# Kernel optimization log

Measured on AMD Instinct MI355X. Metric: run time of the kernel, lower is better.

## Reference

```python
import jax, jax.numpy as jnp
import numpy as np

TOPK = 0.1  # fraction of h*w spatial positions, from __init__ default


def setup_inputs() -> dict:
    key = jax.random.key(0)
    x = jax.random.normal(key, (32, 256, 56, 56), dtype=jnp.float32)
    return {"x": x}


def reference(x) -> jnp.ndarray:
    # Faithful translation of TopKLayer.sparse_hw (including its quirky
    # comparison of ascending *ranks* against the spatial *index* of the
    # k-th largest element, exactly as the torch code does).
    n, c, h, w = x.shape
    k = int(max(1, TOPK * h * w))  # topk_keep_num = 313 for 56x56
    x_r = x.reshape(n * c, h * w)              # (nc, hw)
    abs_x = jnp.abs(x_r)
    # ranks[i, j] = ascending rank of abs_x[i, j] within row i
    ranks = jnp.argsort(jnp.argsort(abs_x, axis=1), axis=1)
    # spatial index of the k-th largest |x| in each row
    thr_idx = jax.lax.top_k(abs_x, k)[1][:, -1]  # (nc,)
    mask = (ranks < thr_idx[:, None]).reshape(n, c, h, w)
    return x * mask.astype(x.dtype)
```

## Files before the change

### kernel.cpp

```cpp
#include <hip/hip_runtime.h>
#include <stdint.h>


#define HW   3136
#define NT   256
#define KSEL 313u
#define NB0  2048
#define SP0  (NB0 / NT)
#define CAP  512

__device__ __forceinline__ unsigned block_scan_incl(unsigned v, unsigned* wt) {
    const int lane = threadIdx.x & 63;
    const int w = threadIdx.x >> 6;
    for (int d = 1; d < 64; d <<= 1) {
        unsigned o = __shfl_up(v, d, 64);
        if (lane >= d) v += o;
    }
    if (lane == 63) wt[w] = v;
    __syncthreads();
    unsigned add = 0;
    for (int i = 0; i < w; ++i) add += wt[i];
    __syncthreads();
    return v + add;
}

template <bool fromTop>
__device__ void locate0(const unsigned* hist, unsigned rank,
                        unsigned* wt, unsigned* s_b) {
    const int t = threadIdx.x;
    const int base = t * SP0;
    unsigned g = 0;
#pragma unroll
    for (int i = 0; i < SP0; ++i) {
        int b = fromTop ? (NB0 - 1 - (base + i)) : (base + i);
        g += hist[b];
    }
    unsigned S = block_scan_incl(g, wt);
    if (S >= rank && (S - g) < rank) {
        unsigned lr = rank - (S - g);
        unsigned acc = 0;
        for (int i = 0; i < SP0; ++i) {
            int b = fromTop ? (NB0 - 1 - (base + i)) : (base + i);
            unsigned h = hist[b];
            acc += h;
            if (acc >= lr) { s_b[0] = (unsigned)b; s_b[1] = lr - (acc - h); break; }
        }
    }
    if (t == 0) s_b[3] = 0;
    __syncthreads();
}

template <bool fromTop>
__device__ void select_stable(const uint4* s_x4, const unsigned* hist0,
                              unsigned* cand, unsigned* wt, unsigned* s_b,
                              unsigned rank, unsigned& keyOut, unsigned& eOut) {
    const int t = threadIdx.x;
    locate0<fromTop>(hist0, rank, wt, s_b);
    const unsigned b0 = s_b[0];
    const unsigned m  = s_b[1];

    for (int j = t; j < HW / 4; j += NT) {
        uint4 v = s_x4[j];
        const unsigned i0 = 4u * (unsigned)j;
        unsigned k;
        k = v.x & 0x7fffffffu;
        if ((k >> 20) == b0) { unsigned p = atomicAdd(&s_b[3], 1u); if (p < CAP) cand[p] = ((k & 0xFFFFFu) << 12) | i0; }
        k = v.y & 0x7fffffffu;
        if ((k >> 20) == b0) { unsigned p = atomicAdd(&s_b[3], 1u); if (p < CAP) cand[p] = ((k & 0xFFFFFu) << 12) | (i0 + 1u); }
        k = v.z & 0x7fffffffu;
        if ((k >> 20) == b0) { unsigned p = atomicAdd(&s_b[3], 1u); if (p < CAP) cand[p] = ((k & 0xFFFFFu) << 12) | (i0 + 2u); }
        k = v.w & 0x7fffffffu;
        if ((k >> 20) == b0) { unsigned p = atomicAdd(&s_b[3], 1u); if (p < CAP) cand[p] = ((k & 0xFFFFFu) << 12) | (i0 + 3u); }
    }
    __syncthreads();
    const unsigned cnt = s_b[3];

    if (cnt <= CAP) {
        for (int i = t; i < (int)cnt; i += NT) {
            const unsigned ci = cand[i];
            const unsigned Ci = fromTop ? (ci ^ 0xFFFu) : ci;
            unsigned r = 1;
            for (int j = 0; j < (int)cnt; ++j) {
                const unsigned Cj = fromTop ? (cand[j] ^ 0xFFFu) : cand[j];
                if (fromTop ? (Cj > Ci) : (Cj < Ci)) r++;
            }
            if (r == m) s_b[2] = ci;
        }
        __syncthreads();
        const unsigned ci = s_b[2];
        keyOut = (b0 << 20) | (ci >> 12);
        eOut = ci & 0xFFFu;
    } else {
        const unsigned* s_x = (const unsigned*)s_x4;
        for (int j = t; j < HW; j += NT) {
            const unsigned k = s_x[j] & 0x7fffffffu;
            if ((k >> 20) != b0) continue;
            unsigned Ci = ((k & 0xFFFFFu) << 12) | (unsigned)j;
            if (fromTop) Ci ^= 0xFFFu;
            unsigned r = 1;
            for (int j2 = 0; j2 < HW; ++j2) {
                const unsigned k2 = s_x[j2] & 0x7fffffffu;
                if ((k2 >> 20) != b0) continue;
                unsigned Cj = ((k2 & 0xFFFFFu) << 12) | (unsigned)j2;
                if (fromTop) Cj ^= 0xFFFu;
                if (fromTop ? (Cj > Ci) : (Cj < Ci)) r++;
            }
            if (r == m) s_b[2] = ((k & 0xFFFFFu) << 12) | (unsigned)j;
        }
        __syncthreads();
        const unsigned ci = s_b[2];
        keyOut = (b0 << 20) | (ci >> 12);
        eOut = ci & 0xFFFu;
    }
}

extern "C" __global__ void __launch_bounds__(NT)
topk_kernel(const float* __restrict__ x, float* __restrict__ out) {
    __shared__ uint4 s_x4[HW / 4];
    __shared__ unsigned s_hist0[NB0];
    __shared__ unsigned s_cand[CAP];
    __shared__ unsigned s_wt[4];
    __shared__ unsigned s_b[4];

    const int t = threadIdx.x;
    const int row = blockIdx.x;
    const uint4* __restrict__ xin = (const uint4*)(x + (size_t)row * HW);
    uint4* __restrict__ xout = (uint4*)(out + (size_t)row * HW);

    for (int i = t; i < NB0; i += NT) s_hist0[i] = 0;
    __syncthreads();
    for (int j = t; j < HW / 4; j += NT) {
        uint4 v = xin[j];
        s_x4[j] = v;
        atomicAdd(&s_hist0[(v.x & 0x7fffffffu) >> 20], 1u);
        atomicAdd(&s_hist0[(v.y & 0x7fffffffu) >> 20], 1u);
        atomicAdd(&s_hist0[(v.z & 0x7fffffffu) >> 20], 1u);
        atomicAdd(&s_hist0[(v.w & 0x7fffffffu) >> 20], 1u);
    }
    __syncthreads();

    unsigned KA, tIdx;
    select_stable<true>(s_x4, s_hist0, s_cand, s_wt, s_b, KSEL, KA, tIdx);

    if (tIdx == 0) {
        uint4 z = make_uint4(0u, 0u, 0u, 0u);
        for (int j = t; j < HW / 4; j += NT) xout[j] = z;
        return;
    }

    unsigned KB, eB;
    select_stable<false>(s_x4, s_hist0, s_cand, s_wt, s_b, tIdx, KB, eB);

    for (int j = t; j < HW / 4; j += NT) {
        uint4 v = s_x4[j];
        const unsigned i0 = 4u * (unsigned)j;
        unsigned k;
        k = v.x & 0x7fffffffu; if (!(k < KB || (k == KB && i0      <= eB))) v.x = 0u;
        k = v.y & 0x7fffffffu; if (!(k < KB || (k == KB && i0 + 1u <= eB))) v.y = 0u;
        k = v.z & 0x7fffffffu; if (!(k < KB || (k == KB && i0 + 2u <= eB))) v.z = 0u;
        k = v.w & 0x7fffffffu; if (!(k < KB || (k == KB && i0 + 3u <= eB))) v.w = 0u;
        xout[j] = v;
    }
}

extern "C" void kernel_launch(void* const* d_in, const int* in_sizes, int n_in,
                              void* d_out, int out_size, void* d_ws, size_t ws_size,
                              hipStream_t stream) {
    const float* x = (const float*)d_in[0];
    float* out = (float*)d_out;
    const int rows = in_sizes[0] / HW;
    topk_kernel<<<dim3(rows), dim3(NT), 0, stream>>>(x, out);
}
```

Before: 71.59 us.

## Process one row per wavefront with packed 16-bit histograms and global re-reads

Each row's selection now runs on a single 64-lane wavefront, with four rows per block, instead of a 256-thread block per row. The row is no longer staged in LDS; global memory is re-read on each pass. Histogram counters are packed as 16-bit pairs with padding, and the selection uses wave-level scans and ballots instead of block barriers, plus a second-level histogram to narrow the candidates. The goal is to remove __syncthreads and cut LDS per row so more rows are in flight. In exchange the input is read from global several times per row.

Result: slower. 97.40 us (+36.1%).

```diff
diff --git a/kernel.cpp b/kernel.cpp
--- a/kernel.cpp
+++ b/kernel.cpp
@@ -2,164 +2,258 @@
 #include <stdint.h>
 
 
-#define HW   3136
-#define NT   256
-#define KSEL 313u
-#define NB0  2048
-#define SP0  (NB0 / NT)
-#define CAP  512
-
-__device__ __forceinline__ unsigned block_scan_incl(unsigned v, unsigned* wt) {
-    const int lane = threadIdx.x & 63;
-    const int w = threadIdx.x >> 6;
+#define HW     3136
+#define NW4    784
+#define WPB    4
+#define NT     256
+#define KSEL   313u
+#define NB0WP  1088
+#define NB2WP  136
+#define CAP    320
+#define CAP2   64
+
+#define OFF_H0   0
+#define OFF_CAND 1088
+#define OFF_H2   1408
+#define OFF_CNT  1544
+#define OFF_SCR  1545
+#define OFF_TINY 1546
+#define WW       1616
+
+#define PADW(w) ((w) + ((w) >> 4))
+
+__device__ __forceinline__ unsigned wscan(unsigned v) {
+    const int lane = threadIdx.x & 63;
+#pragma unroll
     for (int d = 1; d < 64; d <<= 1) {
         unsigned o = __shfl_up(v, d, 64);
         if (lane >= d) v += o;
     }
-    if (lane == 63) wt[w] = v;
-    __syncthreads();
-    unsigned add = 0;
-    for (int i = 0; i < w; ++i) add += wt[i];
-    __syncthreads();
-    return v + add;
+    return v;
+}
+
+__device__ __forceinline__ unsigned h16(const unsigned* h, unsigned bin) {
+    unsigned w = h[PADW(bin >> 1)];
+    return (bin & 1) ? (w >> 16) : (w & 0xFFFFu);
+}
+
+__device__ __forceinline__ void hadd(unsigned* h, unsigned bin) {
+    atomicAdd((unsigned*)&h[PADW(bin >> 1)], (bin & 1) ? 0x10000u : 1u);
+}
+
+template <int SEGW, bool fromTop>
+__device__ void locate(const unsigned* h, unsigned m, unsigned& bOut, unsigned& mOut) {
+    const int lane = threadIdx.x & 63;
+    const int seg = fromTop ? (63 - lane) : lane;
+    unsigned s = 0;
+#pragma unroll
+    for (int i = 0; i < SEGW; ++i) {
+        unsigned w = h[PADW(seg * SEGW + i)];
+        s += (w & 0xFFFFu) + (w >> 16);
+    }
+    unsigned S = wscan(s);
+    unsigned long long bal = __ballot(S >= m);
+    int fl = __ffsll(bal) - 1;
+    unsigned packed = 0;
+    if (lane == fl) {
+        unsigned rem = m - (S - s);
+        unsigned acc = 0;
+        const int nb = SEGW * 2;
+        for (int i = 0; i < nb; ++i) {
+            unsigned bin = fromTop ? (unsigned)(seg * nb + nb - 1 - i)
+                                   : (unsigned)(seg * nb + i);
+            unsigned hh = h16(h, bin);
+            acc += hh;
+            if (acc >= rem) { packed = (bin << 16) | (rem - (acc - hh)); break; }
+        }
+    }
+    packed = __shfl(packed, fl, 64);
+    bOut = packed >> 16;
+    mOut = packed & 0xFFFFu;
+}
+
+__device__ unsigned occ_scan(unsigned* wl, const uint4* xin, unsigned K, unsigned mm) {
+    const int lane = threadIdx.x & 63;
+    unsigned prev = 0;
+    for (int it = 0; it < 13; ++it) {
+        int j = it * 64 + lane;
+        unsigned lm = 0;
+        if (j < NW4) {
+            uint4 v = xin[j];
+            lm  = ((v.x & 0x7fffffffu) == K) ? 1u : 0u;
+            lm |= ((v.y & 0x7fffffffu) == K) ? 2u : 0u;
+            lm |= ((v.z & 0x7fffffffu) == K) ? 4u : 0u;
+            lm |= ((v.w & 0x7fffffffu) == K) ? 8u : 0u;
+        }
+        unsigned c = __popc(lm);
+        unsigned S = wscan(c);
+        unsigned tot = __shfl(S, 63, 64);
+        unsigned ex = prev + S - c;
+        if (lm && ex < mm && mm <= ex + c) {
+            unsigned need = mm - ex, s2 = 0, bit = 0;
+            for (bit = 0; bit < 4; ++bit)
+                if (lm & (1u << bit)) { if (++s2 == need) break; }
+            wl[OFF_SCR] = (unsigned)(j * 4) + bit;
+        }
+        prev += tot;
+        if (prev >= mm) break;
+    }
+    return wl[OFF_SCR];
 }
 
 template <bool fromTop>
-__device__ void locate0(const unsigned* hist, unsigned rank,
-                        unsigned* wt, unsigned* s_b) {
-    const int t = threadIdx.x;
-    const int base = t * SP0;
-    unsigned g = 0;
-#pragma unroll
-    for (int i = 0; i < SP0; ++i) {
-        int b = fromTop ? (NB0 - 1 - (base + i)) : (base + i);
-        g += hist[b];
-    }
-    unsigned S = block_scan_incl(g, wt);
-    if (S >= rank && (S - g) < rank) {
-        unsigned lr = rank - (S - g);
-        unsigned acc = 0;
-        for (int i = 0; i < SP0; ++i) {
-            int b = fromTop ? (NB0 - 1 - (base + i)) : (base + i);
-            unsigned h = hist[b];
-            acc += h;
-            if (acc >= lr) { s_b[0] = (unsigned)b; s_b[1] = lr - (acc - h); break; }
-        }
-    }
-    if (t == 0) s_b[3] = 0;
-    __syncthreads();
+__device__ void refine_level(unsigned* wl, const uint4* xin, unsigned pfx, int pshift,
+                             int bshift, unsigned bmask, unsigned& m, unsigned& dout) {
+    unsigned* h2 = wl + OFF_H2;
+    const int lane = threadIdx.x & 63;
+    for (int i = lane; i < NB2WP; i += 64) h2[i] = 0;
+    for (int it = 0; it < 13; ++it) {
+        int j = it * 64 + lane;
+        if (j < NW4) {
+            uint4 v = xin[j];
+            unsigned k;
+            k = v.x & 0x7fffffffu; if ((k >> pshift) == pfx) hadd(h2, (k >> bshift) & bmask);
+            k = v.y & 0x7fffffffu; if ((k >> pshift) == pfx) hadd(h2, (k >> bshift) & bmask);
+            k = v.z & 0x7fffffffu; if ((k >> pshift) == pfx) hadd(h2, (k >> bshift) & bmask);
+            k = v.w & 0x7fffffffu; if ((k >> pshift) == pfx) hadd(h2, (k >> bshift) & bmask);
+        }
+    }
+    unsigned b2, m2;
+    locate<2, fromTop>(h2, m, b2, m2);
+    dout = b2; m = m2;
 }
 
 template <bool fromTop>
-__device__ void select_stable(const uint4* s_x4, const unsigned* hist0,
-                              unsigned* cand, unsigned* wt, unsigned* s_b,
-                              unsigned rank, unsigned& keyOut, unsigned& eOut) {
-    const int t = threadIdx.x;
-    locate0<fromTop>(hist0, rank, wt, s_b);
-    const unsigned b0 = s_b[0];
-    const unsigned m  = s_b[1];
-
-    for (int j = t; j < HW / 4; j += NT) {
-        uint4 v = s_x4[j];
-        const unsigned i0 = 4u * (unsigned)j;
-        unsigned k;
-        k = v.x & 0x7fffffffu;
-        if ((k >> 20) == b0) { unsigned p = atomicAdd(&s_b[3], 1u); if (p < CAP) cand[p] = ((k & 0xFFFFFu) << 12) | i0; }
-        k = v.y & 0x7fffffffu;
-        if ((k >> 20) == b0) { unsigned p = atomicAdd(&s_b[3], 1u); if (p < CAP) cand[p] = ((k & 0xFFFFFu) << 12) | (i0 + 1u); }
-        k = v.z & 0x7fffffffu;
-        if ((k >> 20) == b0) { unsigned p = atomicAdd(&s_b[3], 1u); if (p < CAP) cand[p] = ((k & 0xFFFFFu) << 12) | (i0 + 2u); }
-        k = v.w & 0x7fffffffu;
-        if ((k >> 20) == b0) { unsigned p = atomicAdd(&s_b[3], 1u); if (p < CAP) cand[p] = ((k & 0xFFFFFu) << 12) | (i0 + 3u); }
-    }
-    __syncthreads();
-    const unsigned cnt = s_b[3];
-
+__device__ bool sel_cand(unsigned* wl, unsigned cnt, unsigned m, unsigned& cOut) {
+    unsigned* h2 = wl + OFF_H2;
+    unsigned* cand = wl + OFF_CAND;
+    const int lane = threadIdx.x & 63;
+    for (int i = lane; i < NB2WP; i += 64) h2[i] = 0;
+    for (int i = lane; i < (int)cnt; i += 64) hadd(h2, cand[i] >> 24);
+    unsigned b2, m2;
+    locate<2, fromTop>(h2, m, b2, m2);
+    if (lane == 0) wl[OFF_SCR] = 0;
+    for (int i = lane; i < (int)cnt; i += 64) {
+        unsigned c = cand[i];
+        if ((c >> 24) == b2) {
+            unsigned p = atomicAdd((unsigned*)&wl[OFF_SCR], 1u);
+            if (p < CAP2) wl[OFF_TINY + p] = c;
+        }
+    }
+    unsigned c2 = wl[OFF_SCR];
+    if (c2 > CAP2) return false;
+    unsigned res = wl[OFF_TINY];
+    if (c2 > 1) {
+        if (lane == 0) {
+            for (unsigned i = 0; i < c2; ++i) {
+                unsigned ci = wl[OFF_TINY + i];
+                unsigned di = fromTop ? (ci ^ 0xFFFu) : ci;
+                unsigned r = 1;
+                for (unsigned jj = 0; jj < c2; ++jj) {
+                    unsigned dj = fromTop ? (wl[OFF_TINY + jj] ^ 0xFFFu) : wl[OFF_TINY + jj];
+                    if (fromTop ? (dj > di) : (dj < di)) r++;
+                }
+                if (r == m2) res = ci;
+            }
+        }
+        res = __shfl(res, 0, 64);
+    }
+    cOut = res;
+    return true;
+}
+
+template <bool fromTop>
+__device__ void wave_select(unsigned* wl, const uint4* xin, unsigned m,
+                            unsigned& keyOut, unsigned& eOut) {
+    const int lane = threadIdx.x & 63;
+    unsigned b0, m1;
+    locate<16, fromTop>(wl + OFF_H0, m, b0, m1);
+    if (lane == 0) wl[OFF_CNT] = 0;
+    unsigned* cand = wl + OFF_CAND;
+    for (int it = 0; it < 13; ++it) {
+        int j = it * 64 + lane;
+        if (j < NW4) {
+            uint4 v = xin[j];
+            unsigned i0 = 4u * (unsigned)j;
+            unsigned k, p;
+            k = v.x & 0x7fffffffu;
+            if ((k >> 20) == b0) { p = atomicAdd((unsigned*)&wl[OFF_CNT], 1u); if (p < CAP) cand[p] = ((k & 0xFFFFFu) << 12) | i0; }
+            k = v.y & 0x7fffffffu;
+            if ((k >> 20) == b0) { p = atomicAdd((unsigned*)&wl[OFF_CNT], 1u); if (p < CAP) cand[p] = ((k & 0xFFFFFu) << 12) | (i0 + 1u); }
+            k = v.z & 0x7fffffffu;
+            if ((k >> 20) == b0) { p = atomicAdd((unsigned*)&wl[OFF_CNT], 1u); if (p < CAP) cand[p] = ((k & 0xFFFFFu) << 12) | (i0 + 2u); }
+            k = v.w & 0x7fffffffu;
+            if ((k >> 20) == b0) { p = atomicAdd((unsigned*)&wl[OFF_CNT], 1u); if (p < CAP) cand[p] = ((k & 0xFFFFFu) << 12) | (i0 + 3u); }
+        }
+    }
+    unsigned cnt = wl[OFF_CNT];
     if (cnt <= CAP) {
-        for (int i = t; i < (int)cnt; i += NT) {
-            const unsigned ci = cand[i];
-            const unsigned Ci = fromTop ? (ci ^ 0xFFFu) : ci;
-            unsigned r = 1;
-            for (int j = 0; j < (int)cnt; ++j) {
-                const unsigned Cj = fromTop ? (cand[j] ^ 0xFFFu) : cand[j];
-                if (fromTop ? (Cj > Ci) : (Cj < Ci)) r++;
-            }
-            if (r == m) s_b[2] = ci;
-        }
-        __syncthreads();
-        const unsigned ci = s_b[2];
-        keyOut = (b0 << 20) | (ci >> 12);
-        eOut = ci & 0xFFFu;
-    } else {
-        const unsigned* s_x = (const unsigned*)s_x4;
-        for (int j = t; j < HW; j += NT) {
-            const unsigned k = s_x[j] & 0x7fffffffu;
-            if ((k >> 20) != b0) continue;
-            unsigned Ci = ((k & 0xFFFFFu) << 12) | (unsigned)j;
-            if (fromTop) Ci ^= 0xFFFu;
-            unsigned r = 1;
-            for (int j2 = 0; j2 < HW; ++j2) {
-                const unsigned k2 = s_x[j2] & 0x7fffffffu;
-                if ((k2 >> 20) != b0) continue;
-                unsigned Cj = ((k2 & 0xFFFFFu) << 12) | (unsigned)j2;
-                if (fromTop) Cj ^= 0xFFFu;
-                if (fromTop ? (Cj > Ci) : (Cj < Ci)) r++;
-            }
-            if (r == m) s_b[2] = ((k & 0xFFFFFu) << 12) | (unsigned)j;
-        }
-        __syncthreads();
-        const unsigned ci = s_b[2];
-        keyOut = (b0 << 20) | (ci >> 12);
-        eOut = ci & 0xFFFu;
-    }
+        unsigned c;
+        if (sel_cand<fromTop>(wl, cnt, m1, c)) {
+            keyOut = (b0 << 20) | (c >> 12);
+            eOut = c & 0xFFFu;
+            return;
+        }
+    }
+    unsigned d1, d2, d3, mm = m1;
+    refine_level<fromTop>(wl, xin, b0, 20, 12, 0xFFu, mm, d1);
+    refine_level<fromTop>(wl, xin, (b0 << 8) | d1, 12, 4, 0xFFu, mm, d2);
+    refine_level<fromTop>(wl, xin, (b0 << 16) | (d1 << 8) | d2, 4, 0, 0xFu, mm, d3);
+    unsigned K = (((b0 << 16) | (d1 << 8) | d2) << 4) | d3;
+    keyOut = K;
+    eOut = occ_scan(wl, xin, K, mm);
 }
 
 extern "C" __global__ void __launch_bounds__(NT)
 topk_kernel(const float* __restrict__ x, float* __restrict__ out) {
-    __shared__ uint4 s_x4[HW / 4];
-    __shared__ unsigned s_hist0[NB0];
-    __shared__ unsigned s_cand[CAP];
-    __shared__ unsigned s_wt[4];
-    __shared__ unsigned s_b[4];
-
-    const int t = threadIdx.x;
-    const int row = blockIdx.x;
+    __shared__ unsigned lds[WPB * WW];
+    const int lane = threadIdx.x & 63;
+    const int wid = threadIdx.x >> 6;
+    const int row = blockIdx.x * WPB + wid;
+    unsigned* wl = lds + wid * WW;
     const uint4* __restrict__ xin = (const uint4*)(x + (size_t)row * HW);
     uint4* __restrict__ xout = (uint4*)(out + (size_t)row * HW);
 
-    for (int i = t; i < NB0; i += NT) s_hist0[i] = 0;
-    __syncthreads();
-    for (int j = t; j < HW / 4; j += NT) {
-        uint4 v = xin[j];
-        s_x4[j] = v;
-        atomicAdd(&s_hist0[(v.x & 0x7fffffffu) >> 20], 1u);
-        atomicAdd(&s_hist0[(v.y & 0x7fffffffu) >> 20], 1u);
-        atomicAdd(&s_hist0[(v.z & 0x7fffffffu) >> 20], 1u);
-        atomicAdd(&s_hist0[(v.w & 0x7fffffffu) >> 20], 1u);
-    }
-    __syncthreads();
+    unsigned* h0 = wl + OFF_H0;
+    for (int i = lane; i < NB0WP; i += 64) h0[i] = 0;
+    for (int it = 0; it < 13; ++it) {
+        int j = it * 64 + lane;
+        if (j < NW4) {
+            uint4 v = xin[j];
+            hadd(h0, (v.x & 0x7fffffffu) >> 20);
+            hadd(h0, (v.y & 0x7fffffffu) >> 20);
+            hadd(h0, (v.z & 0x7fffffffu) >> 20);
+            hadd(h0, (v.w & 0x7fffffffu) >> 20);
+        }
+    }
 
     unsigned KA, tIdx;
-    select_stable<true>(s_x4, s_hist0, s_cand, s_wt, s_b, KSEL, KA, tIdx);
+    wave_select<true>(wl, xin, KSEL, KA, tIdx);
 
     if (tIdx == 0) {
         uint4 z = make_uint4(0u, 0u, 0u, 0u);
-        for (int j = t; j < HW / 4; j += NT) xout[j] = z;
+        for (int it = 0; it < 13; ++it) {
+            int j = it * 64 + lane;
+            if (j < NW4) xout[j] = z;
+        }
         return;
     }
 
     unsigned KB, eB;
-    select_stable<false>(s_x4, s_hist0, s_cand, s_wt, s_b, tIdx, KB, eB);
-
-    for (int j = t; j < HW / 4; j += NT) {
-        uint4 v = s_x4[j];
-        const unsigned i0 = 4u * (unsigned)j;
-        unsigned k;
-        k = v.x & 0x7fffffffu; if (!(k < KB || (k == KB && i0      <= eB))) v.x = 0u;
-        k = v.y & 0x7fffffffu; if (!(k < KB || (k == KB && i0 + 1u <= eB))) v.y = 0u;
-        k = v.z & 0x7fffffffu; if (!(k < KB || (k == KB && i0 + 2u <= eB))) v.z = 0u;
-        k = v.w & 0x7fffffffu; if (!(k < KB || (k == KB && i0 + 3u <= eB))) v.w = 0u;
-        xout[j] = v;
+    wave_select<false>(wl, xin, tIdx, KB, eB);
+
+    for (int it = 0; it < 13; ++it) {
+        int j = it * 64 + lane;
+        if (j < NW4) {
+            uint4 v = xin[j];
+            unsigned i0 = 4u * (unsigned)j;
+            unsigned k;
+            k = v.x & 0x7fffffffu; if (!(k < KB || (k == KB && i0      <= eB))) v.x = 0u;
+            k = v.y & 0x7fffffffu; if (!(k < KB || (k == KB && i0 + 1u <= eB))) v.y = 0u;
+            k = v.z & 0x7fffffffu; if (!(k < KB || (k == KB && i0 + 2u <= eB))) v.z = 0u;
+            k = v.w & 0x7fffffffu; if (!(k < KB || (k == KB && i0 + 3u <= eB))) v.w = 0u;
+            xout[j] = v;
+        }
     }
 }
 
@@ -169,5 +263,5 @@
     const float* x = (const float*)d_in[0];
     float* out = (float*)d_out;
     const int rows = in_sizes[0] / HW;
-    topk_kernel<<<dim3(rows), dim3(NT), 0, stream>>>(x, out);
-}
+    topk_kernel<<<dim3(rows / WPB), dim3(NT), 0, stream>>>(x, out);
+}
```
